# Optimization experiments

Hardware: AMD Instinct MI355X
Metric: run time of the kernel (lower is better)

The kernel has to match this reference:

```python
import jax, jax.numpy as jnp
import numpy as np

HOURS = 24
SU, SL, TU, TL = 100.0, 0.0, 100.0, 0.0
N, M, L, E = 32, 128, 128, 128
T_DIM, U_DIM, L_DIM = 25, 2000, 10000


def setup_inputs() -> dict:
    key = jax.random.key(0)
    ks = jax.random.split(key, 18)
    s = 0.02
    full_seq = jax.random.randint(ks[0], (N, M), 1, L_DIM)
    time_seq = jax.random.randint(ks[1], (N, M), 1, 720)
    user = jax.random.randint(ks[2], (N,), 1, U_DIM)
    posneg = jax.random.randint(ks[3], (N, L), 1, L_DIM)
    traj_len = jax.random.randint(ks[4], (N,), 1, M + 1)
    mat1 = jax.random.uniform(ks[5], (N, M, M, 2), dtype=jnp.float32) * 100.0
    mat2 = jax.random.uniform(ks[6], (N, M, L), dtype=jnp.float32) * 100.0
    vec = jax.random.uniform(ks[7], (N, M), dtype=jnp.float32) * 100.0
    def tab(k, n):  # embedding table with padding_idx=0 zeroed
        return (jax.random.normal(k, (n, E), dtype=jnp.float32) * s).at[0].set(0.0)
    emb_t = tab(ks[8], T_DIM)
    emb_u = tab(ks[9], U_DIM)
    emb_loc = tab(ks[10], L_DIM)
    emb_sl = tab(ks[11], 2)
    emb_su = tab(ks[12], 2)
    emb_tl = tab(ks[13], 2)
    emb_tu = tab(ks[14], 2)
    Wq = jax.random.normal(ks[15], (E, E), dtype=jnp.float32) * s
    Wk = jax.random.normal(ks[16], (E, E), dtype=jnp.float32) * s
    Wv = jax.random.normal(ks[17], (E, E), dtype=jnp.float32) * s
    return dict(full_seq=full_seq, time_seq=time_seq, user=user, posneg=posneg,
                traj_len=traj_len, mat1=mat1, mat2=mat2, vec=vec,
                emb_t=emb_t, emb_u=emb_u, emb_loc=emb_loc,
                emb_sl=emb_sl, emb_su=emb_su, emb_tl=emb_tl, emb_tu=emb_tu,
                Wq=Wq, Wk=Wk, Wv=Wv)


def _interval(e_l, e_u, d, lo, hi):
    # (e_l*(hi-d) + e_u*(d-lo)) / (hi-lo); e_* are [...,E], d is [...]
    return (e_l * (hi - d)[..., None] + e_u * (d - lo)[..., None]) / (hi - lo)


def reference(full_seq, time_seq, user, posneg, traj_len, mat1, mat2, vec,
              emb_t, emb_u, emb_loc, emb_sl, emb_su, emb_tl, emb_tu, Wq, Wk, Wv):
    n, m = full_seq.shape
    tim = (time_seq - 1) % HOURS + 1
    joint = emb_t[tim] + emb_loc[full_seq] + emb_u[user][:, None, :]  # [N,M,E]

    # --- stage 1: self-attention with spatiotemporal relative bias ---
    delta_s, delta_t = mat1[..., 0], mat1[..., 1]  # [N,M,M]
    valid = (jnp.arange(m)[None, :] < traj_len[:, None]).astype(jnp.int32)  # [N,M]
    mask2d = valid[:, None, :] * valid[:, :, None]  # [N,M,M] in {0,1}
    delta = (_interval(emb_sl[mask2d], emb_su[mask2d], delta_s, SL, SU)
             + _interval(emb_tl[mask2d], emb_tu[mask2d], delta_t, TL, TU)).sum(-1)
    fmask = mask2d.astype(joint.dtype)
    q = joint @ Wq.T
    k = joint @ Wk.T
    v = joint @ Wv.T
    attn = jax.nn.softmax(jnp.einsum('bme,bne->bmn', q, k) + delta, axis=-1) * fmask
    self_attn = jnp.einsum('bmn,bne->bme', attn, v)  # [N,M,E]

    # --- stage 2: candidate attention ---
    mask1 = valid[:, :, None]  # [N,M,1]
    sp = _interval(emb_sl[mask1], emb_su[mask1], mat2, SL, SU)            # [N,M,L,E]
    tm = _interval(emb_tl[mask1], emb_tu[mask1], vec[:, :, None], TL, TU)  # [N,M,1,E]
    self_delta = jnp.swapaxes((sp + tm).sum(-1), -1, -2)  # [N,L,M]
    cand = emb_loc[posneg]  # [N,L,E]
    attn2 = jnp.einsum('ble,bme->blm', cand, self_attn) * self_delta
    return attn2.sum(-1)  # [N,L]
```

## Files before the change

### kernel.cpp

```cpp
#include <hip/hip_runtime.h>
#include <hip/hip_bf16.h>

#define HOURS 24
#define NB 32
#define MM 128
#define EE 128

typedef short bf16x8 __attribute__((ext_vector_type(8)));
typedef float f32x4 __attribute__((ext_vector_type(4)));

__device__ __forceinline__ unsigned short f2bfu(float f) {
    __hip_bfloat16 h = __float2bfloat16(f);
    return __builtin_bit_cast(unsigned short, h);
}
__device__ __forceinline__ unsigned int pack2(float a, float b) {
    return (unsigned int)f2bfu(a) | ((unsigned int)f2bfu(b) << 16);
}
__device__ __forceinline__ int swz8(int row, int unit) {
    return row * 128 + (((unit ^ (row & 7)) & 15) << 3);
}

__global__ __launch_bounds__(256) void k_qkv(
    const int* __restrict__ time_seq, const int* __restrict__ full_seq,
    const int* __restrict__ user,
    const float* __restrict__ emb_t, const float* __restrict__ emb_u,
    const float* __restrict__ emb_loc,
    const float* __restrict__ Wq, const float* __restrict__ Wk, const float* __restrict__ Wv,
    short* __restrict__ qws, short* __restrict__ kws, short* __restrict__ vtws)
{
    __shared__ alignas(16) short Wl[128 * 128];
    __shared__ alignas(16) short Jl[64 * 128];
    int b = blockIdx.y;
    int which = blockIdx.x >> 1;
    int half = blockIdx.x & 1;
    int m0 = half * 64;
    int tid = threadIdx.x;
    const float* W = (which == 0) ? Wq : (which == 1) ? Wk : Wv;

    const float4* W4 = (const float4*)W;
#pragma unroll
    for (int it = 0; it < 16; ++it) {
        int i4 = it * 256 + tid;
        float4 v = W4[i4];
        int n = i4 >> 5;
        int e = (i4 & 31) << 2;
        uint2 pk;
        pk.x = pack2(v.x, v.y);
        pk.y = pack2(v.z, v.w);
        *(uint2*)&Wl[swz8(n, e >> 3) + (e & 7)] = pk;
    }
    int uid = user[b];
    const float4* Eu4 = (const float4*)(emb_u + (size_t)uid * 128);
#pragma unroll
    for (int it = 0; it < 8; ++it) {
        int i4 = it * 256 + tid;
        int mm = i4 >> 5;
        int e = (i4 & 31) << 2;
        int m = m0 + mm;
        int t = time_seq[b * MM + m];
        int tim = (t - 1) % HOURS + 1;
        int loc = full_seq[b * MM + m];
        float4 a = ((const float4*)(emb_t + (size_t)tim * 128))[e >> 2];
        float4 c = ((const float4*)(emb_loc + (size_t)loc * 128))[e >> 2];
        float4 u = Eu4[e >> 2];
        uint2 pk;
        pk.x = pack2(a.x + c.x + u.x, a.y + c.y + u.y);
        pk.y = pack2(a.z + c.z + u.z, a.w + c.w + u.w);
        *(uint2*)&Jl[swz8(mm, e >> 3) + (e & 7)] = pk;
    }
    __syncthreads();

    int l = tid & 63, w = tid >> 6;
    int lr = l & 15, lg = l >> 4;

    if (which < 2) {
        bf16x8 af[2][4];
#pragma unroll
        for (int nt = 0; nt < 2; ++nt) {
            int n = (2 * w + nt) * 16 + lr;
#pragma unroll
            for (int kf = 0; kf < 4; ++kf)
                af[nt][kf] = *(const bf16x8*)&Wl[swz8(n, kf * 4 + lg)];
        }
        f32x4 acc[2][4];
#pragma unroll
        for (int nt = 0; nt < 2; ++nt)
#pragma unroll
            for (int mt = 0; mt < 4; ++mt) acc[nt][mt] = (f32x4){0.f, 0.f, 0.f, 0.f};
#pragma unroll
        for (int mt = 0; mt < 4; ++mt) {
            int m = mt * 16 + lr;
            bf16x8 bf[4];
#pragma unroll
            for (int kf = 0; kf < 4; ++kf)
                bf[kf] = *(const bf16x8*)&Jl[swz8(m, kf * 4 + lg)];
#pragma unroll
            for (int nt = 0; nt < 2; ++nt)
#pragma unroll
                for (int kf = 0; kf < 4; ++kf)
                    acc[nt][mt] = __builtin_amdgcn_mfma_f32_16x16x32_bf16(af[nt][kf], bf[kf], acc[nt][mt], 0, 0, 0);
        }
        short* outp = (which == 0) ? qws : kws;
#pragma unroll
        for (int nt = 0; nt < 2; ++nt)
#pragma unroll
            for (int mt = 0; mt < 4; ++mt) {
                int mg = m0 + mt * 16 + lr;
                int n0 = (2 * w + nt) * 16 + lg * 4;
                f32x4 a = acc[nt][mt];
                uint2 pk;
                pk.x = pack2(a[0], a[1]);
                pk.y = pack2(a[2], a[3]);
                *(uint2*)&outp[(size_t)(b * MM + mg) * EE + n0] = pk;
            }
    } else {
        bf16x8 bfr[2][4];
#pragma unroll
        for (int nt = 0; nt < 2; ++nt) {
            int n = (2 * w + nt) * 16 + lr;
#pragma unroll
            for (int kf = 0; kf < 4; ++kf)
                bfr[nt][kf] = *(const bf16x8*)&Wl[swz8(n, kf * 4 + lg)];
        }
        f32x4 acc[4][2];
#pragma unroll
        for (int mt = 0; mt < 4; ++mt)
#pragma unroll
            for (int nt = 0; nt < 2; ++nt) acc[mt][nt] = (f32x4){0.f, 0.f, 0.f, 0.f};
#pragma unroll
        for (int mt = 0; mt < 4; ++mt) {
            int m = mt * 16 + lr;
            bf16x8 af[4];
#pragma unroll
            for (int kf = 0; kf < 4; ++kf)
                af[kf] = *(const bf16x8*)&Jl[swz8(m, kf * 4 + lg)];
#pragma unroll
            for (int nt = 0; nt < 2; ++nt)
#pragma unroll
                for (int kf = 0; kf < 4; ++kf)
                    acc[mt][nt] = __builtin_amdgcn_mfma_f32_16x16x32_bf16(af[kf], bfr[nt][kf], acc[mt][nt], 0, 0, 0);
        }
#pragma unroll
        for (int mt = 0; mt < 4; ++mt)
#pragma unroll
            for (int nt = 0; nt < 2; ++nt) {
                int ng = (2 * w + nt) * 16 + lr;
                int mp = m0 + mt * 16 + lg * 4;
                f32x4 a = acc[mt][nt];
                uint2 pk;
                pk.x = pack2(a[0], a[1]);
                pk.y = pack2(a[2], a[3]);
                *(uint2*)&vtws[(size_t)(b * MM + ng) * MM + mp] = pk;
            }
    }
}

__global__ __launch_bounds__(256) void k_attn(
    const short* __restrict__ qws, const short* __restrict__ kws,
    const short* __restrict__ vtws,
    const float* __restrict__ mat1, const int* __restrict__ traj_len,
    const float* __restrict__ esl, const float* __restrict__ esu,
    const float* __restrict__ etl, const float* __restrict__ etu,
    short* __restrict__ saws)
{
    __shared__ alignas(16) short Kl[128 * 128];
    __shared__ alignas(16) short VTl[128 * 128];
    __shared__ alignas(16) short Pl[16 * 128];
    __shared__ alignas(16) float Sl[16][132];
    __shared__ float coef[8];

    int b = blockIdx.y;
    int chunk = blockIdx.x;
    int i0 = chunk * 16;
    int tid = threadIdx.x;
    int l = tid & 63, w = tid >> 6;
    int lr = l & 15, lg = l >> 4;
    int tl = traj_len[b];

    {
        const float* tb[4] = {esl, esu, etl, etu};
#pragma unroll
        for (int s = 0; s < 2; ++s) {
            int c = 2 * w + s;
            const float* t = tb[c >> 1];
            float v = t[(c & 1) * 128 + l] + t[(c & 1) * 128 + 64 + l];
#pragma unroll
            for (int off = 32; off >= 1; off >>= 1) v += __shfl_xor(v, off, 64);
            if (l == 0) coef[c] = v;
        }
    }
    const uint4* K4 = (const uint4*)(kws + (size_t)b * MM * EE);
    const uint4* VT4 = (const uint4*)(vtws + (size_t)b * MM * MM);
#pragma unroll
    for (int it = 0; it < 8; ++it) {
        int U = it * 256 + tid;
        int r = U >> 4, u = U & 15;
        *(uint4*)&Kl[swz8(r, u)] = K4[U];
    }
#pragma unroll
    for (int it = 0; it < 8; ++it) {
        int U = it * 256 + tid;
        int r = U >> 4, u = U & 15;
        *(uint4*)&VTl[swz8(r, u)] = VT4[U];
    }
    bf16x8 qf[4];
#pragma unroll
    for (int kf = 0; kf < 4; ++kf)
        qf[kf] = *(const bf16x8*)&qws[(size_t)(b * MM + i0 + lr) * EE + kf * 32 + lg * 8];
    __syncthreads();

    f32x4 accs[2];
#pragma unroll
    for (int t2 = 0; t2 < 2; ++t2) accs[t2] = (f32x4){0.f, 0.f, 0.f, 0.f};
#pragma unroll
    for (int t2 = 0; t2 < 2; ++t2) {
        int j = (2 * w + t2) * 16 + lr;
#pragma unroll
        for (int kf = 0; kf < 4; ++kf) {
            bf16x8 bf = *(const bf16x8*)&Kl[swz8(j, kf * 4 + lg)];
            accs[t2] = __builtin_amdgcn_mfma_f32_16x16x32_bf16(qf[kf], bf, accs[t2], 0, 0, 0);
        }
    }
#pragma unroll
    for (int t2 = 0; t2 < 2; ++t2) {
        int jc = (2 * w + t2) * 16 + lr;
#pragma unroll
        for (int r = 0; r < 4; ++r) Sl[lg * 4 + r][jc] = accs[t2][r];
    }
    __syncthreads();

    {
        int r16 = tid >> 4, u = tid & 15;
        int j0 = u * 8;
        int i = i0 + r16;
        int mi = (i < tl) ? 1 : 0;
        float c0_1 = coef[1] + coef[5];
        float c1_1 = (coef[3] - coef[1]) * 0.01f;
        float c2_1 = (coef[7] - coef[5]) * 0.01f;
        float c0_0 = coef[0] + coef[4];
        float c1_0 = (coef[2] - coef[0]) * 0.01f;
        float c2_0 = (coef[6] - coef[4]) * 0.01f;
        float4 s01 = *(float4*)&Sl[r16][j0];
        float4 s23 = *(float4*)&Sl[r16][j0 + 4];
        float sv[8] = {s01.x, s01.y, s01.z, s01.w, s23.x, s23.y, s23.z, s23.w};
        const float4* m14 = (const float4*)(mat1 + (size_t)(b * MM + i) * MM * 2 + j0 * 2);
        float4 d0 = m14[0], d1 = m14[1], d2 = m14[2], d3 = m14[3];
        float ds[8] = {d0.x, d0.z, d1.x, d1.z, d2.x, d2.z, d3.x, d3.z};
        float dt[8] = {d0.y, d0.w, d1.y, d1.w, d2.y, d2.w, d3.y, d3.w};
        float lgv[8];
        int mk[8];
#pragma unroll
        for (int jj = 0; jj < 8; ++jj) {
            int j = j0 + jj;
            mk[jj] = mi & ((j < tl) ? 1 : 0);
            float cc0 = mk[jj] ? c0_1 : c0_0;
            float cc1 = mk[jj] ? c1_1 : c1_0;
            float cc2 = mk[jj] ? c2_1 : c2_0;
            lgv[jj] = sv[jj] + cc0 + cc1 * ds[jj] + cc2 * dt[jj];
        }
        float mx = lgv[0];
#pragma unroll
        for (int jj = 1; jj < 8; ++jj) mx = fmaxf(mx, lgv[jj]);
#pragma unroll
        for (int off = 8; off >= 1; off >>= 1) mx = fmaxf(mx, __shfl_xor(mx, off, 64));
        float ee[8], sum = 0.f;
#pragma unroll
        for (int jj = 0; jj < 8; ++jj) { ee[jj] = __expf(lgv[jj] - mx); sum += ee[jj]; }
#pragma unroll
        for (int off = 8; off >= 1; off >>= 1) sum += __shfl_xor(sum, off, 64);
        float inv = 1.0f / sum;
        float p[8];
#pragma unroll
        for (int jj = 0; jj < 8; ++jj) p[jj] = ee[jj] * inv * (float)mk[jj];
        uint4 pk;
        pk.x = pack2(p[0], p[1]);
        pk.y = pack2(p[2], p[3]);
        pk.z = pack2(p[4], p[5]);
        pk.w = pack2(p[6], p[7]);
        *(uint4*)&Pl[swz8(r16, u)] = pk;
    }
    __syncthreads();

    bf16x8 bp[4];
#pragma unroll
    for (int kf = 0; kf < 4; ++kf)
        bp[kf] = *(const bf16x8*)&Pl[swz8(lr, kf * 4 + lg)];
    f32x4 accv[2];
#pragma unroll
    for (int t2 = 0; t2 < 2; ++t2) accv[t2] = (f32x4){0.f, 0.f, 0.f, 0.f};
#pragma unroll
    for (int t2 = 0; t2 < 2; ++t2) {
        int e = (2 * w + t2) * 16 + lr;
#pragma unroll
        for (int kf = 0; kf < 4; ++kf) {
            bf16x8 af = *(const bf16x8*)&VTl[swz8(e, kf * 4 + lg)];
            accv[t2] = __builtin_amdgcn_mfma_f32_16x16x32_bf16(af, bp[kf], accv[t2], 0, 0, 0);
        }
    }
#pragma unroll
    for (int t2 = 0; t2 < 2; ++t2) {
        int ig = i0 + lr;
        int e0 = (2 * w + t2) * 16 + lg * 4;
        f32x4 a = accv[t2];
        uint2 pk;
        pk.x = pack2(a[0], a[1]);
        pk.y = pack2(a[2], a[3]);
        *(uint2*)&saws[(size_t)(b * MM + ig) * EE + e0] = pk;
    }
}

__global__ __launch_bounds__(256) void k_final(
    const short* __restrict__ saws, const int* __restrict__ posneg,
    const float* __restrict__ emb_loc, const float* __restrict__ mat2,
    const float* __restrict__ vecg, const int* __restrict__ traj_len,
    const float* __restrict__ esl, const float* __restrict__ esu,
    const float* __restrict__ etl, const float* __restrict__ etu,
    float* __restrict__ outp)
{
    __shared__ alignas(16) short SAl[128 * 128];
    __shared__ alignas(16) short CAl[32 * 128];
    __shared__ alignas(16) float M2l[128 * 36];
    __shared__ float TMS[128];
    __shared__ float BSV[128];
    __shared__ float PART[2][32];
    __shared__ float coef[8];

    int b = blockIdx.y;
    int l0 = blockIdx.x * 32;
    int tid = threadIdx.x;
    int l = tid & 63, w = tid >> 6;
    int lr = l & 15, lg = l >> 4;
    int tl = traj_len[b];

    {
        const float* tb[4] = {esl, esu, etl, etu};
#pragma unroll
        for (int s = 0; s < 2; ++s) {
            int c = 2 * w + s;
            const float* t = tb[c >> 1];
            float v = t[(c & 1) * 128 + l] + t[(c & 1) * 128 + 64 + l];
#pragma unroll
            for (int off = 32; off >= 1; off >>= 1) v += __shfl_xor(v, off, 64);
            if (l == 0) coef[c] = v;
        }
    }
    const uint4* SA4 = (const uint4*)(saws + (size_t)b * MM * EE);
#pragma unroll
    for (int it = 0; it < 8; ++it) {
        int U = it * 256 + tid;
        int r = U >> 4, u = U & 15;
        *(uint4*)&SAl[swz8(r, u)] = SA4[U];
    }
#pragma unroll
    for (int it = 0; it < 4; ++it) {
        int i4 = it * 256 + tid;
        int lrow = i4 >> 5;
        int e = (i4 & 31) << 2;
        int p = posneg[b * MM + l0 + lrow];
        float4 v = ((const float4*)(emb_loc + (size_t)p * 128))[e >> 2];
        uint2 pk;
        pk.x = pack2(v.x, v.y);
        pk.y = pack2(v.z, v.w);
        *(uint2*)&CAl[swz8(lrow, e >> 3) + (e & 7)] = pk;
    }
#pragma unroll
    for (int it = 0; it < 4; ++it) {
        int i4 = it * 256 + tid;
        int m = i4 >> 3;
        int c = (i4 & 7) << 2;
        float4 v = ((const float4*)(mat2 + (size_t)(b * MM + m) * MM + l0))[c >> 2];
        *(float4*)&M2l[m * 36 + c] = v;
    }
    __syncthreads();

    if (tid < 128) {
        int vv = (tid < tl) ? 1 : 0;
        float ssl = vv ? coef[1] : coef[0];
        float ssu = vv ? coef[3] : coef[2];
        float stl = vv ? coef[5] : coef[4];
        float stu = vv ? coef[7] : coef[6];
        TMS[tid] = ssl + stl + (stu - stl) * 0.01f * vecg[b * MM + tid];
        BSV[tid] = (ssu - ssl) * 0.01f;
    }

    int ltile = w & 1, mhalf = w >> 1;
    bf16x8 ca[4];
#pragma unroll
    for (int kf = 0; kf < 4; ++kf)
        ca[kf] = *(const bf16x8*)&CAl[swz8(ltile * 16 + lr, kf * 4 + lg)];
    f32x4 acc[4];
#pragma unroll
    for (int mt = 0; mt < 4; ++mt) acc[mt] = (f32x4){0.f, 0.f, 0.f, 0.f};
#pragma unroll
    for (int mt = 0; mt < 4; ++mt) {
        int m = (mhalf * 4 + mt) * 16 + lr;
#pragma unroll
        for (int kf = 0; kf < 4; ++kf) {
            bf16x8 bf = *(const bf16x8*)&SAl[swz8(m, kf * 4 + lg)];
            acc[mt] = __builtin_amdgcn_mfma_f32_16x16x32_bf16(ca[kf], bf, acc[mt], 0, 0, 0);
        }
    }
    __syncthreads();

#pragma unroll
    for (int r = 0; r < 4; ++r) {
        int lrel = ltile * 16 + lg * 4 + r;
        float vs = 0.f;
#pragma unroll
        for (int mt = 0; mt < 4; ++mt) {
            int m = (mhalf * 4 + mt) * 16 + lr;
            vs += acc[mt][r] * (TMS[m] + BSV[m] * M2l[m * 36 + lrel]);
        }
#pragma unroll
        for (int off = 8; off >= 1; off >>= 1) vs += __shfl_xor(vs, off, 64);
        if (lr == 0) PART[mhalf][lrel] = vs;
    }
    __syncthreads();
    if (tid < 32) outp[b * MM + l0 + tid] = PART[0][tid] + PART[1][tid];
}

extern "C" void kernel_launch(void* const* d_in, const int* in_sizes, int n_in,
                              void* d_out, int out_size, void* d_ws, size_t ws_size,
                              hipStream_t stream) {
    const int* full_seq = (const int*)d_in[0];
    const int* time_seq = (const int*)d_in[1];
    const int* user     = (const int*)d_in[2];
    const int* posneg   = (const int*)d_in[3];
    const int* traj_len = (const int*)d_in[4];
    const float* mat1   = (const float*)d_in[5];
    const float* mat2   = (const float*)d_in[6];
    const float* vec    = (const float*)d_in[7];
    const float* emb_t  = (const float*)d_in[8];
    const float* emb_u  = (const float*)d_in[9];
    const float* emb_loc= (const float*)d_in[10];
    const float* emb_sl = (const float*)d_in[11];
    const float* emb_su = (const float*)d_in[12];
    const float* emb_tl = (const float*)d_in[13];
    const float* emb_tu = (const float*)d_in[14];
    const float* Wq     = (const float*)d_in[15];
    const float* Wk     = (const float*)d_in[16];
    const float* Wv     = (const float*)d_in[17];

    short* qws  = (short*)d_ws;
    short* kws  = qws + (size_t)NB * MM * EE;
    short* vtws = kws + (size_t)NB * MM * EE;
    short* saws = vtws + (size_t)NB * MM * EE;

    k_qkv<<<dim3(6, 32), 256, 0, stream>>>(time_seq, full_seq, user,
                                           emb_t, emb_u, emb_loc,
                                           Wq, Wk, Wv, qws, kws, vtws);
    k_attn<<<dim3(8, 32), 256, 0, stream>>>(qws, kws, vtws, mat1, traj_len,
                                            emb_sl, emb_su, emb_tl, emb_tu, saws);
    k_final<<<dim3(4, 32), 256, 0, stream>>>(saws, posneg, emb_loc, mat2, vec,
                                             traj_len, emb_sl, emb_su, emb_tl, emb_tu,
                                             (float*)d_out);
}
```

Before: 24.17 us.

## Load MFMA operands directly from global memory instead of staging in LDS

Removes the LDS staging of weights in k_qkv, of K and V^T in k_attn, and of SA, candidate embeddings and mat2 in k_final. MFMA fragments are now read straight from global or L2 memory. k_final is also re-tiled to 16 candidates per block, doubling its grid, and each wave reduces its own partial sums. The goal is to cut the LDS fill traffic, barriers and shared-memory footprint so that occupancy rises, at the cost of uncoalesced 16-byte fragment loads and more redundant global reads across blocks.

```diff
diff --git a/kernel.cpp b/kernel.cpp
--- a/kernel.cpp
+++ b/kernel.cpp
@@ -19,6 +19,16 @@
 __device__ __forceinline__ int swz8(int row, int unit) {
     return row * 128 + (((unit ^ (row & 7)) & 15) << 3);
 }
+__device__ __forceinline__ bf16x8 load_w_frag(const float* base) {
+    float4 x = *(const float4*)base;
+    float4 y = *(const float4*)(base + 4);
+    union { unsigned int u[4]; bf16x8 v; } r;
+    r.u[0] = pack2(x.x, x.y); r.u[1] = pack2(x.z, x.w);
+    r.u[2] = pack2(y.x, y.y); r.u[3] = pack2(y.z, y.w);
+    return r.v;
+}
+
+#define MFMA(a, b, c) __builtin_amdgcn_mfma_f32_16x16x32_bf16(a, b, c, 0, 0, 0)
 
 __global__ __launch_bounds__(256) void k_qkv(
     const int* __restrict__ time_seq, const int* __restrict__ full_seq,
@@ -28,59 +38,46 @@
     const float* __restrict__ Wq, const float* __restrict__ Wk, const float* __restrict__ Wv,
     short* __restrict__ qws, short* __restrict__ kws, short* __restrict__ vtws)
 {
-    __shared__ alignas(16) short Wl[128 * 128];
     __shared__ alignas(16) short Jl[64 * 128];
     int b = blockIdx.y;
     int which = blockIdx.x >> 1;
     int half = blockIdx.x & 1;
     int m0 = half * 64;
     int tid = threadIdx.x;
-    const float* W = (which == 0) ? Wq : (which == 1) ? Wk : Wv;
-
-    const float4* W4 = (const float4*)W;
-#pragma unroll
-    for (int it = 0; it < 16; ++it) {
-        int i4 = it * 256 + tid;
-        float4 v = W4[i4];
-        int n = i4 >> 5;
-        int e = (i4 & 31) << 2;
-        uint2 pk;
-        pk.x = pack2(v.x, v.y);
-        pk.y = pack2(v.z, v.w);
-        *(uint2*)&Wl[swz8(n, e >> 3) + (e & 7)] = pk;
-    }
+    int l = tid & 63, w = tid >> 6;
+    int lr = l & 15, lg = l >> 4;
+
     int uid = user[b];
     const float4* Eu4 = (const float4*)(emb_u + (size_t)uid * 128);
 #pragma unroll
     for (int it = 0; it < 8; ++it) {
         int i4 = it * 256 + tid;
         int mm = i4 >> 5;
-        int e = (i4 & 31) << 2;
+        int fq = i4 & 31;
         int m = m0 + mm;
         int t = time_seq[b * MM + m];
         int tim = (t - 1) % HOURS + 1;
         int loc = full_seq[b * MM + m];
-        float4 a = ((const float4*)(emb_t + (size_t)tim * 128))[e >> 2];
-        float4 c = ((const float4*)(emb_loc + (size_t)loc * 128))[e >> 2];
-        float4 u = Eu4[e >> 2];
+        float4 a = ((const float4*)(emb_t + (size_t)tim * 128))[fq];
+        float4 c = ((const float4*)(emb_loc + (size_t)loc * 128))[fq];
+        float4 u = Eu4[fq];
         uint2 pk;
         pk.x = pack2(a.x + c.x + u.x, a.y + c.y + u.y);
         pk.y = pack2(a.z + c.z + u.z, a.w + c.w + u.w);
-        *(uint2*)&Jl[swz8(mm, e >> 3) + (e & 7)] = pk;
-    }
-    __syncthreads();
-
-    int l = tid & 63, w = tid >> 6;
-    int lr = l & 15, lg = l >> 4;
+        *(uint2*)&Jl[swz8(mm, fq >> 1) + (fq & 1) * 4] = pk;
+    }
+    __syncthreads();
 
     if (which < 2) {
+        const float* W = which ? Wk : Wq;
+        short* outp = which ? kws : qws;
         bf16x8 af[2][4];
 #pragma unroll
         for (int nt = 0; nt < 2; ++nt) {
             int n = (2 * w + nt) * 16 + lr;
 #pragma unroll
             for (int kf = 0; kf < 4; ++kf)
-                af[nt][kf] = *(const bf16x8*)&Wl[swz8(n, kf * 4 + lg)];
+                af[nt][kf] = load_w_frag(W + (size_t)n * 128 + kf * 32 + lg * 8);
         }
         f32x4 acc[2][4];
 #pragma unroll
@@ -89,28 +86,25 @@
             for (int mt = 0; mt < 4; ++mt) acc[nt][mt] = (f32x4){0.f, 0.f, 0.f, 0.f};
 #pragma unroll
         for (int mt = 0; mt < 4; ++mt) {
-            int m = mt * 16 + lr;
             bf16x8 bf[4];
 #pragma unroll
             for (int kf = 0; kf < 4; ++kf)
-                bf[kf] = *(const bf16x8*)&Jl[swz8(m, kf * 4 + lg)];
+                bf[kf] = *(const bf16x8*)&Jl[swz8(mt * 16 + lr, kf * 4 + lg)];
 #pragma unroll
             for (int nt = 0; nt < 2; ++nt)
 #pragma unroll
                 for (int kf = 0; kf < 4; ++kf)
-                    acc[nt][mt] = __builtin_amdgcn_mfma_f32_16x16x32_bf16(af[nt][kf], bf[kf], acc[nt][mt], 0, 0, 0);
-        }
-        short* outp = (which == 0) ? qws : kws;
+                    acc[nt][mt] = MFMA(af[nt][kf], bf[kf], acc[nt][mt]);
+        }
 #pragma unroll
         for (int nt = 0; nt < 2; ++nt)
 #pragma unroll
             for (int mt = 0; mt < 4; ++mt) {
                 int mg = m0 + mt * 16 + lr;
                 int n0 = (2 * w + nt) * 16 + lg * 4;
-                f32x4 a = acc[nt][mt];
                 uint2 pk;
-                pk.x = pack2(a[0], a[1]);
-                pk.y = pack2(a[2], a[3]);
+                pk.x = pack2(acc[nt][mt][0], acc[nt][mt][1]);
+                pk.y = pack2(acc[nt][mt][2], acc[nt][mt][3]);
                 *(uint2*)&outp[(size_t)(b * MM + mg) * EE + n0] = pk;
             }
     } else {
@@ -120,7 +114,7 @@
             int n = (2 * w + nt) * 16 + lr;
 #pragma unroll
             for (int kf = 0; kf < 4; ++kf)
-                bfr[nt][kf] = *(const bf16x8*)&Wl[swz8(n, kf * 4 + lg)];
+                bfr[nt][kf] = load_w_frag(Wv + (size_t)n * 128 + kf * 32 + lg * 8);
         }
         f32x4 acc[4][2];
 #pragma unroll
@@ -129,16 +123,15 @@
             for (int nt = 0; nt < 2; ++nt) acc[mt][nt] = (f32x4){0.f, 0.f, 0.f, 0.f};
 #pragma unroll
         for (int mt = 0; mt < 4; ++mt) {
-            int m = mt * 16 + lr;
             bf16x8 af[4];
 #pragma unroll
             for (int kf = 0; kf < 4; ++kf)
-                af[kf] = *(const bf16x8*)&Jl[swz8(m, kf * 4 + lg)];
+                af[kf] = *(const bf16x8*)&Jl[swz8(mt * 16 + lr, kf * 4 + lg)];
 #pragma unroll
             for (int nt = 0; nt < 2; ++nt)
 #pragma unroll
                 for (int kf = 0; kf < 4; ++kf)
-                    acc[mt][nt] = __builtin_amdgcn_mfma_f32_16x16x32_bf16(af[kf], bfr[nt][kf], acc[mt][nt], 0, 0, 0);
+                    acc[mt][nt] = MFMA(af[kf], bfr[nt][kf], acc[mt][nt]);
         }
 #pragma unroll
         for (int mt = 0; mt < 4; ++mt)
@@ -146,10 +139,9 @@
             for (int nt = 0; nt < 2; ++nt) {
                 int ng = (2 * w + nt) * 16 + lr;
                 int mp = m0 + mt * 16 + lg * 4;
-                f32x4 a = acc[mt][nt];
                 uint2 pk;
-                pk.x = pack2(a[0], a[1]);
-                pk.y = pack2(a[2], a[3]);
+                pk.x = pack2(acc[mt][nt][0], acc[mt][nt][1]);
+                pk.y = pack2(acc[mt][nt][2], acc[mt][nt][3]);
                 *(uint2*)&vtws[(size_t)(b * MM + ng) * MM + mp] = pk;
             }
     }
@@ -163,15 +155,12 @@
     const float* __restrict__ etl, const float* __restrict__ etu,
     short* __restrict__ saws)
 {
-    __shared__ alignas(16) short Kl[128 * 128];
-    __shared__ alignas(16) short VTl[128 * 128];
+    __shared__ alignas(16) float Sf[16 * 132];
     __shared__ alignas(16) short Pl[16 * 128];
-    __shared__ alignas(16) float Sl[16][132];
     __shared__ float coef[8];
 
     int b = blockIdx.y;
-    int chunk = blockIdx.x;
-    int i0 = chunk * 16;
+    int i0 = blockIdx.x * 16;
     int tid = threadIdx.x;
     int l = tid & 63, w = tid >> 6;
     int lr = l & 15, lg = l >> 4;
@@ -189,43 +178,23 @@
             if (l == 0) coef[c] = v;
         }
     }
-    const uint4* K4 = (const uint4*)(kws + (size_t)b * MM * EE);
-    const uint4* VT4 = (const uint4*)(vtws + (size_t)b * MM * MM);
-#pragma unroll
-    for (int it = 0; it < 8; ++it) {
-        int U = it * 256 + tid;
-        int r = U >> 4, u = U & 15;
-        *(uint4*)&Kl[swz8(r, u)] = K4[U];
-    }
-#pragma unroll
-    for (int it = 0; it < 8; ++it) {
-        int U = it * 256 + tid;
-        int r = U >> 4, u = U & 15;
-        *(uint4*)&VTl[swz8(r, u)] = VT4[U];
-    }
     bf16x8 qf[4];
 #pragma unroll
     for (int kf = 0; kf < 4; ++kf)
         qf[kf] = *(const bf16x8*)&qws[(size_t)(b * MM + i0 + lr) * EE + kf * 32 + lg * 8];
-    __syncthreads();
-
-    f32x4 accs[2];
-#pragma unroll
-    for (int t2 = 0; t2 < 2; ++t2) accs[t2] = (f32x4){0.f, 0.f, 0.f, 0.f};
+
 #pragma unroll
     for (int t2 = 0; t2 < 2; ++t2) {
-        int j = (2 * w + t2) * 16 + lr;
+        int jt = 2 * w + t2;
+        f32x4 acc = (f32x4){0.f, 0.f, 0.f, 0.f};
 #pragma unroll
         for (int kf = 0; kf < 4; ++kf) {
-            bf16x8 bf = *(const bf16x8*)&Kl[swz8(j, kf * 4 + lg)];
-            accs[t2] = __builtin_amdgcn_mfma_f32_16x16x32_bf16(qf[kf], bf, accs[t2], 0, 0, 0);
-        }
-    }
-#pragma unroll
-    for (int t2 = 0; t2 < 2; ++t2) {
-        int jc = (2 * w + t2) * 16 + lr;
-#pragma unroll
-        for (int r = 0; r < 4; ++r) Sl[lg * 4 + r][jc] = accs[t2][r];
+            bf16x8 bf = *(const bf16x8*)&kws[(size_t)(b * MM + jt * 16 + lr) * EE + kf * 32 + lg * 8];
+            acc = MFMA(qf[kf], bf, acc);
+        }
+#pragma unroll
+        for (int r = 0; r < 4; ++r)
+            Sf[(lg * 4 + r) * 132 + jt * 16 + lr] = acc[r];
     }
     __syncthreads();
 
@@ -240,10 +209,11 @@
         float c0_0 = coef[0] + coef[4];
         float c1_0 = (coef[2] - coef[0]) * 0.01f;
         float c2_0 = (coef[6] - coef[4]) * 0.01f;
-        float4 s01 = *(float4*)&Sl[r16][j0];
-        float4 s23 = *(float4*)&Sl[r16][j0 + 4];
+        const float* sb = &Sf[r16 * 132 + j0];
+        float4 s01 = *(const float4*)sb;
+        float4 s23 = *(const float4*)(sb + 4);
         float sv[8] = {s01.x, s01.y, s01.z, s01.w, s23.x, s23.y, s23.z, s23.w};
-        const float4* m14 = (const float4*)(mat1 + (size_t)(b * MM + i) * MM * 2 + j0 * 2);
+        const float4* m14 = (const float4*)(mat1 + ((size_t)(b * MM + i) * MM + j0) * 2);
         float4 d0 = m14[0], d1 = m14[1], d2 = m14[2], d3 = m14[3];
         float ds[8] = {d0.x, d0.z, d1.x, d1.z, d2.x, d2.z, d3.x, d3.z};
         float dt[8] = {d0.y, d0.w, d1.y, d1.w, d2.y, d2.w, d3.y, d3.w};
@@ -269,14 +239,11 @@
 #pragma unroll
         for (int off = 8; off >= 1; off >>= 1) sum += __shfl_xor(sum, off, 64);
         float inv = 1.0f / sum;
-        float p[8];
-#pragma unroll
-        for (int jj = 0; jj < 8; ++jj) p[jj] = ee[jj] * inv * (float)mk[jj];
         uint4 pk;
-        pk.x = pack2(p[0], p[1]);
-        pk.y = pack2(p[2], p[3]);
-        pk.z = pack2(p[4], p[5]);
-        pk.w = pack2(p[6], p[7]);
+        pk.x = pack2(ee[0] * inv * mk[0], ee[1] * inv * mk[1]);
+        pk.y = pack2(ee[2] * inv * mk[2], ee[3] * inv * mk[3]);
+        pk.z = pack2(ee[4] * inv * mk[4], ee[5] * inv * mk[5]);
+        pk.w = pack2(ee[6] * inv * mk[6], ee[7] * inv * mk[7]);
         *(uint4*)&Pl[swz8(r16, u)] = pk;
     }
     __syncthreads();
@@ -285,26 +252,20 @@
 #pragma unroll
     for (int kf = 0; kf < 4; ++kf)
         bp[kf] = *(const bf16x8*)&Pl[swz8(lr, kf * 4 + lg)];
-    f32x4 accv[2];
-#pragma unroll
-    for (int t2 = 0; t2 < 2; ++t2) accv[t2] = (f32x4){0.f, 0.f, 0.f, 0.f};
 #pragma unroll
     for (int t2 = 0; t2 < 2; ++t2) {
-        int e = (2 * w + t2) * 16 + lr;
+        int et = 2 * w + t2;
+        f32x4 acc = (f32x4){0.f, 0.f, 0.f, 0.f};
 #pragma unroll
         for (int kf = 0; kf < 4; ++kf) {
-            bf16x8 af = *(const bf16x8*)&VTl[swz8(e, kf * 4 + lg)];
-            accv[t2] = __builtin_amdgcn_mfma_f32_16x16x32_bf16(af, bp[kf], accv[t2], 0, 0, 0);
-        }
-    }
-#pragma unroll
-    for (int t2 = 0; t2 < 2; ++t2) {
+            bf16x8 af = *(const bf16x8*)&vtws[(size_t)(b * MM + et * 16 + lr) * MM + kf * 32 + lg * 8];
+            acc = MFMA(af, bp[kf], acc);
+        }
         int ig = i0 + lr;
-        int e0 = (2 * w + t2) * 16 + lg * 4;
-        f32x4 a = accv[t2];
+        int e0 = et * 16 + lg * 4;
         uint2 pk;
-        pk.x = pack2(a[0], a[1]);
-        pk.y = pack2(a[2], a[3]);
+        pk.x = pack2(acc[0], acc[1]);
+        pk.y = pack2(acc[2], acc[3]);
         *(uint2*)&saws[(size_t)(b * MM + ig) * EE + e0] = pk;
     }
 }
@@ -317,16 +278,12 @@
     const float* __restrict__ etl, const float* __restrict__ etu,
     float* __restrict__ outp)
 {
-    __shared__ alignas(16) short SAl[128 * 128];
-    __shared__ alignas(16) short CAl[32 * 128];
-    __shared__ alignas(16) float M2l[128 * 36];
-    __shared__ float TMS[128];
-    __shared__ float BSV[128];
-    __shared__ float PART[2][32];
     __shared__ float coef[8];
+    __shared__ float tms[128], bsv[128];
+    __shared__ float PART[4][16];
 
     int b = blockIdx.y;
-    int l0 = blockIdx.x * 32;
+    int l0 = blockIdx.x * 16;
     int tid = threadIdx.x;
     int l = tid & 63, w = tid >> 6;
     int lr = l & 15, lg = l >> 4;
@@ -344,33 +301,11 @@
             if (l == 0) coef[c] = v;
         }
     }
-    const uint4* SA4 = (const uint4*)(saws + (size_t)b * MM * EE);
-#pragma unroll
-    for (int it = 0; it < 8; ++it) {
-        int U = it * 256 + tid;
-        int r = U >> 4, u = U & 15;
-        *(uint4*)&SAl[swz8(r, u)] = SA4[U];
-    }
-#pragma unroll
-    for (int it = 0; it < 4; ++it) {
-        int i4 = it * 256 + tid;
-        int lrow = i4 >> 5;
-        int e = (i4 & 31) << 2;
-        int p = posneg[b * MM + l0 + lrow];
-        float4 v = ((const float4*)(emb_loc + (size_t)p * 128))[e >> 2];
-        uint2 pk;
-        pk.x = pack2(v.x, v.y);
-        pk.y = pack2(v.z, v.w);
-        *(uint2*)&CAl[swz8(lrow, e >> 3) + (e & 7)] = pk;
-    }
-#pragma unroll
-    for (int it = 0; it < 4; ++it) {
-        int i4 = it * 256 + tid;
-        int m = i4 >> 3;
-        int c = (i4 & 7) << 2;
-        float4 v = ((const float4*)(mat2 + (size_t)(b * MM + m) * MM + l0))[c >> 2];
-        *(float4*)&M2l[m * 36 + c] = v;
-    }
+    int p = posneg[b * MM + l0 + lr];
+    bf16x8 caf[4];
+#pragma unroll
+    for (int kf = 0; kf < 4; ++kf)
+        caf[kf] = load_w_frag(emb_loc + (size_t)p * 128 + kf * 32 + lg * 8);
     __syncthreads();
 
     if (tid < 128) {
@@ -379,44 +314,41 @@
         float ssu = vv ? coef[3] : coef[2];
         float stl = vv ? coef[5] : coef[4];
         float stu = vv ? coef[7] : coef[6];
-        TMS[tid] = ssl + stl + (stu - stl) * 0.01f * vecg[b * MM + tid];
-        BSV[tid] = (ssu - ssl) * 0.01f;
-    }
-
-    int ltile = w & 1, mhalf = w >> 1;
-    bf16x8 ca[4];
-#pragma unroll
-    for (int kf = 0; kf < 4; ++kf)
-        ca[kf] = *(const bf16x8*)&CAl[swz8(ltile * 16 + lr, kf * 4 + lg)];
-    f32x4 acc[4];
-#pragma unroll
-    for (int mt = 0; mt < 4; ++mt) acc[mt] = (f32x4){0.f, 0.f, 0.f, 0.f};
-#pragma unroll
-    for (int mt = 0; mt < 4; ++mt) {
-        int m = (mhalf * 4 + mt) * 16 + lr;
+        tms[tid] = ssl + stl + (stu - stl) * 0.01f * vecg[b * MM + tid];
+        bsv[tid] = (ssu - ssl) * 0.01f;
+    }
+    __syncthreads();
+
+    float vout[4] = {0.f, 0.f, 0.f, 0.f};
+#pragma unroll
+    for (int t2 = 0; t2 < 2; ++t2) {
+        int mt = 2 * w + t2;
+        f32x4 acc = (f32x4){0.f, 0.f, 0.f, 0.f};
 #pragma unroll
         for (int kf = 0; kf < 4; ++kf) {
-            bf16x8 bf = *(const bf16x8*)&SAl[swz8(m, kf * 4 + lg)];
-            acc[mt] = __builtin_amdgcn_mfma_f32_16x16x32_bf16(ca[kf], bf, acc[mt], 0, 0, 0);
-        }
-    }
-    __syncthreads();
-
+            bf16x8 bf = *(const bf16x8*)&saws[(size_t)(b * MM + mt * 16 + lr) * EE + kf * 32 + lg * 8];
+            acc = MFMA(caf[kf], bf, acc);
+        }
+        int mloc = mt * 16 + lr;
+        float wt = tms[mloc], wb = bsv[mloc];
+        float4 m2 = *(const float4*)&mat2[(size_t)(b * MM + mloc) * MM + l0 + lg * 4];
+        vout[0] += acc[0] * (wt + wb * m2.x);
+        vout[1] += acc[1] * (wt + wb * m2.y);
+        vout[2] += acc[2] * (wt + wb * m2.z);
+        vout[3] += acc[3] * (wt + wb * m2.w);
+    }
 #pragma unroll
     for (int r = 0; r < 4; ++r) {
-        int lrel = ltile * 16 + lg * 4 + r;
-        float vs = 0.f;
-#pragma unroll
-        for (int mt = 0; mt < 4; ++mt) {
-            int m = (mhalf * 4 + mt) * 16 + lr;
-            vs += acc[mt][r] * (TMS[m] + BSV[m] * M2l[m * 36 + lrel]);
-        }
-#pragma unroll
-        for (int off = 8; off >= 1; off >>= 1) vs += __shfl_xor(vs, off, 64);
-        if (lr == 0) PART[mhalf][lrel] = vs;
-    }
-    __syncthreads();
-    if (tid < 32) outp[b * MM + l0 + tid] = PART[0][tid] + PART[1][tid];
+        float v = vout[r];
+        v += __shfl_xor(v, 1, 64);
+        v += __shfl_xor(v, 2, 64);
+        v += __shfl_xor(v, 4, 64);
+        v += __shfl_xor(v, 8, 64);
+        if (lr == 0) PART[w][lg * 4 + r] = v;
+    }
+    __syncthreads();
+    if (tid < 16)
+        outp[b * MM + l0 + tid] = PART[0][tid] + PART[1][tid] + PART[2][tid] + PART[3][tid];
 }
 
 extern "C" void kernel_launch(void* const* d_in, const int* in_sizes, int n_in,
@@ -451,7 +383,7 @@
                                            Wq, Wk, Wv, qws, kws, vtws);
     k_attn<<<dim3(8, 32), 256, 0, stream>>>(qws, kws, vtws, mat1, traj_len,
                                             emb_sl, emb_su, emb_tl, emb_tu, saws);
-    k_final<<<dim3(4, 32), 256, 0, stream>>>(saws, posneg, emb_loc, mat2, vec,
+    k_final<<<dim3(8, 32), 256, 0, stream>>>(saws, posneg, emb_loc, mat2, vec,
                                              traj_len, emb_sl, emb_su, emb_tl, emb_tu,
                                              (float*)d_out);
 }
```

New measurement: 25.58 us. 5.8% more time.
